# Optimization experiments

Hardware: AMD Instinct MI355X
Metric: run time of the kernel (lower is better)

## Reference

```python
import jax, jax.numpy as jnp
import numpy as np

N_ATOM = 10000
D = 256
N_EDGE = 160000
BN_EPS = 1e-6


def _bn_eval(x, g, b, m, v):
    # BatchNorm1d in eval mode
    return (x - m) * jax.lax.rsqrt(v + BN_EPS) * g + b


def setup_inputs() -> dict:
    key = jax.random.key(0)
    ks = jax.random.split(key, 12)
    def glorot(k, shape):
        fan_in = shape[-1]
        return jax.random.normal(k, shape, dtype=jnp.float32) / np.sqrt(fan_in)
    inp = {
        'atom': jax.random.normal(ks[0], (N_ATOM, D), dtype=jnp.float32),
        'bond_index': jax.random.randint(ks[1], (2, N_EDGE), 0, N_ATOM, dtype=jnp.int32),
        # align: Linear(2D -> 1) + BN(1)
        'W_align': glorot(ks[2], (1, 2 * D)),
        'b_align': jnp.zeros((1,), jnp.float32),
        'bn_a_g': jnp.ones((1,), jnp.float32),
        'bn_a_b': jnp.zeros((1,), jnp.float32),
        'bn_a_m': jnp.zeros((1,), jnp.float32),
        'bn_a_v': jnp.ones((1,), jnp.float32),
        # attend: Linear(D -> D) + BN(D)
        'W_att': glorot(ks[3], (D, D)),
        'b_att': jnp.zeros((D,), jnp.float32),
        'bn_t_g': jnp.ones((D,), jnp.float32),
        'bn_t_b': jnp.zeros((D,), jnp.float32),
        'bn_t_m': jnp.zeros((D,), jnp.float32),
        'bn_t_v': jnp.ones((D,), jnp.float32),
        # GRUCell(D, D): weights stacked [r; z; n] as in torch
        'W_ih': glorot(ks[4], (3 * D, D)),
        'W_hh': glorot(ks[5], (3 * D, D)),
        'b_ih': jnp.zeros((3 * D,), jnp.float32),
        'b_hh': jnp.zeros((3 * D,), jnp.float32),
    }
    return inp


def reference(atom, bond_index, W_align, b_align, bn_a_g, bn_a_b, bn_a_m, bn_a_v,
              W_att, b_att, bn_t_g, bn_t_b, bn_t_m, bn_t_v,
              W_ih, W_hh, b_ih, b_hh):
    num_atom = atom.shape[0]
    src = bond_index[0]
    dst = bond_index[1]

    # gather + concat: [E, 2D]
    feat_align = jnp.concatenate([atom[src], atom[dst]], axis=-1)
    # align score: Linear(2D->1) + BN + leaky_relu -> [E, 1]
    s = feat_align @ W_align.T + b_align
    s = _bn_eval(s, bn_a_g, bn_a_b, bn_a_m, bn_a_v)
    s = jax.nn.leaky_relu(s, negative_slope=0.01)

    # segment softmax over edges grouped by src atom
    seg_max = jax.ops.segment_max(s, src, num_segments=num_atom)  # [N, 1]
    e = jnp.exp(s - seg_max[src])
    denom = jax.ops.segment_sum(e, src, num_segments=num_atom)    # [N, 1]
    attn = e / (denom[src] + 1e-8)                                # [E, 1]

    # attend: Linear(D->D) + BN on gathered dst features
    h = atom[dst] @ W_att.T + b_att
    h = _bn_eval(h, bn_t_g, bn_t_b, bn_t_m, bn_t_v)

    # weighted scatter-add aggregation -> [N, D], then ELU
    context = jax.ops.segment_sum(attn * h, src, num_segments=num_atom)
    context = jax.nn.elu(context)

    # GRUCell: input=context, hidden=atom
    gi = context @ W_ih.T + b_ih   # [N, 3D]
    gh = atom @ W_hh.T + b_hh      # [N, 3D]
    i_r, i_z, i_n = jnp.split(gi, 3, axis=-1)
    h_r, h_z, h_n = jnp.split(gh, 3, axis=-1)
    r = jax.nn.sigmoid(i_r + h_r)
    z = jax.nn.sigmoid(i_z + h_z)
    n = jnp.tanh(i_n + r * h_n)
    update = (1.0 - z) * n + z * atom
    return update
```

## Files before the change

### kernel.cpp

```cpp
#include <hip/hip_runtime.h>
#include <hip/hip_bf16.h>

#define D 256
#define CAP 64

typedef __attribute__((ext_vector_type(8))) short bf16x8;
typedef __attribute__((ext_vector_type(4))) short s16x4;
typedef __attribute__((ext_vector_type(4))) float f32x4;

#define MFMA __builtin_amdgcn_mfma_f32_16x16x32_bf16

__device__ __forceinline__ float s2f(short u) {
    union { unsigned int i; float f; } c;
    c.i = ((unsigned int)(unsigned short)u) << 16;
    return c.f;
}
__device__ __forceinline__ short f2s(float f) {
    union { float f; unsigned int u; } c; c.f = f;
    unsigned int u = c.u;
    u += 0x7fffu + ((u >> 16) & 1u);
    return (short)(u >> 16);
}

__global__ __launch_bounds__(256) void prep_kernel(
    const float* __restrict__ atom, short* __restrict__ atom_bf,
    const float* __restrict__ W_align, const float* __restrict__ b_align,
    const float* __restrict__ g, const float* __restrict__ bb,
    const float* __restrict__ mn, const float* __restrict__ vr,
    float* __restrict__ p0p, float* __restrict__ p1p,
    const float* __restrict__ Wa, short* __restrict__ Wa_bf,
    const float* __restrict__ Wi, short* __restrict__ Wi_bf,
    const float* __restrict__ Wh, short* __restrict__ Wh_bf,
    int* __restrict__ cnt,
    int N, int NROWB, int WCVTB)
{
    int b = blockIdx.x, tid = threadIdx.x;
    if (b < NROWB) {
        int wave = tid >> 6, lane = tid & 63;
        int row = b * 4 + wave;
        if (row >= N) return;
        float4 a = *(const float4*)(atom + (size_t)row * D + lane * 4);
        s16x4 o; o[0] = f2s(a.x); o[1] = f2s(a.y); o[2] = f2s(a.z); o[3] = f2s(a.w);
        ((s16x4*)(atom_bf + (size_t)row * D))[lane] = o;
        float4 w0 = *(const float4*)(W_align + lane * 4);
        float4 w1 = *(const float4*)(W_align + D + lane * 4);
        float d0 = a.x * w0.x + a.y * w0.y + a.z * w0.z + a.w * w0.w;
        float d1 = a.x * w1.x + a.y * w1.y + a.z * w1.z + a.w * w1.w;
        #pragma unroll
        for (int s = 32; s > 0; s >>= 1) {
            d0 += __shfl_xor(d0, s, 64);
            d1 += __shfl_xor(d1, s, 64);
        }
        if (lane == 0) {
            float A = rsqrtf(vr[0] + 1e-6f) * g[0];
            p0p[row] = A * (d0 + b_align[0]) + bb[0] - A * mn[0];
            p1p[row] = A * d1;
        }
        return;
    }
    b -= NROWB;
    if (b < WCVTB) {
        int nW4 = D * D / 4, nG4 = 3 * D * D / 4;
        int j = b * 256 + tid;
        const float* srcp; short* dstp;
        if (j < nW4) { srcp = Wa; dstp = Wa_bf; }
        else { j -= nW4;
            if (j < nG4) { srcp = Wi; dstp = Wi_bf; }
            else { j -= nG4;
                if (j < nG4) { srcp = Wh; dstp = Wh_bf; }
                else return;
            }
        }
        float4 v = ((const float4*)srcp)[j];
        s16x4 o; o[0] = f2s(v.x); o[1] = f2s(v.y); o[2] = f2s(v.z); o[3] = f2s(v.w);
        ((s16x4*)dstp)[j] = o;
        return;
    }
    b -= WCVTB;
    int i = b * 256 + tid;
    if (i < N) cnt[i] = 0;
}

__global__ __launch_bounds__(256) void fill_hA_kernel(
    const int* __restrict__ src, const int* __restrict__ dst,
    int* __restrict__ cnt, int* __restrict__ dlist, int E, int EB,
    const short* __restrict__ atom_bf, const short* __restrict__ W_bf,
    const float* __restrict__ bias,
    const float* __restrict__ g, const float* __restrict__ bb,
    const float* __restrict__ mn, const float* __restrict__ vr,
    short* __restrict__ hA, int N, int NB)
{
    int tid = threadIdx.x;
    if ((int)blockIdx.x < EB) {
        int e = blockIdx.x * 256 + tid;
        if (e < E) {
            int s = src[e];
            int p = atomicAdd(&cnt[s], 1);
            if (p < CAP) dlist[(s << 6) + p] = dst[e];
        }
        return;
    }
    __shared__ short Bs[2048 * 8];
    int bi = blockIdx.x - EB;
    int xcd = bi & 7, rest = bi >> 3;
    int cb = rest & 3, gh = rest >> 2;
    int gg = gh * 8 + xcd;
    if (gg >= NB) return;
    int c0 = cb * 64;
    for (int c = tid; c < 2048; c += 256) {
        int l15c = c & 15, quadc = (c >> 4) & 3, t2 = c >> 6;
        int kkc = t2 & 7, jc = t2 >> 3;
        bf16x8 v = *(const bf16x8*)(W_bf + (size_t)(c0 + jc * 16 + l15c) * D + quadc * 8 + kkc * 32);
        *(bf16x8*)(&Bs[c * 8]) = v;
    }
    __syncthreads();

    int wave = tid >> 6, lane = tid & 63;
    int quad = lane >> 4, l15 = lane & 15;
    int m0 = gg * 128 + wave * 16;
    int ar0 = m0 + l15;       if (ar0 > N - 1) ar0 = N - 1;
    int ar1 = m0 + 64 + l15;  if (ar1 > N - 1) ar1 = N - 1;
    const short* ap0 = atom_bf + (size_t)ar0 * D + quad * 8;
    const short* ap1 = atom_bf + (size_t)ar1 * D + quad * 8;
    const short* lb = &Bs[lane * 8];
    f32x4 acc[2][4];
    #pragma unroll
    for (int t = 0; t < 2; t++)
        #pragma unroll
        for (int j = 0; j < 4; j++) acc[t][j] = (f32x4){0,0,0,0};
    #pragma unroll
    for (int kk = 0; kk < 8; kk++) {
        int k = kk * 32;
        bf16x8 a0 = *(const bf16x8*)(ap0 + k);
        bf16x8 a1 = *(const bf16x8*)(ap1 + k);
        bf16x8 b0 = *(const bf16x8*)(lb + (0 * 8 + kk) * 512);
        bf16x8 b1 = *(const bf16x8*)(lb + (1 * 8 + kk) * 512);
        bf16x8 b2 = *(const bf16x8*)(lb + (2 * 8 + kk) * 512);
        bf16x8 b3 = *(const bf16x8*)(lb + (3 * 8 + kk) * 512);
        acc[0][0] = MFMA(a0, b0, acc[0][0], 0, 0, 0);
        acc[0][1] = MFMA(a0, b1, acc[0][1], 0, 0, 0);
        acc[0][2] = MFMA(a0, b2, acc[0][2], 0, 0, 0);
        acc[0][3] = MFMA(a0, b3, acc[0][3], 0, 0, 0);
        acc[1][0] = MFMA(a1, b0, acc[1][0], 0, 0, 0);
        acc[1][1] = MFMA(a1, b1, acc[1][1], 0, 0, 0);
        acc[1][2] = MFMA(a1, b2, acc[1][2], 0, 0, 0);
        acc[1][3] = MFMA(a1, b3, acc[1][3], 0, 0, 0);
    }
    #pragma unroll
    for (int j = 0; j < 4; j++) {
        int col = c0 + j * 16 + l15;
        float sc = rsqrtf(vr[col] + 1e-6f) * g[col];
        float sh = bb[col] - mn[col] * sc;
        float bi_ = bias[col];
        #pragma unroll
        for (int t = 0; t < 2; t++) {
            #pragma unroll
            for (int r = 0; r < 4; r++) {
                int row = m0 + t * 64 + quad * 4 + r;
                if (row < N) hA[(size_t)row * D + col] = f2s((acc[t][j][r] + bi_) * sc + sh);
            }
        }
    }
}

__global__ __launch_bounds__(256) void agg_kernel(
    const int* __restrict__ cnt, const int* __restrict__ dlist,
    const float* __restrict__ p0p, const float* __restrict__ p1p,
    const short* __restrict__ hA, short* __restrict__ ctx, int N)
{
    int w = (blockIdx.x * blockDim.x + threadIdx.x) >> 6;
    int lane = threadIdx.x & 63;
    if (w >= N) return;
    int deg = cnt[w]; if (deg > CAP) deg = CAP;
    int base = w << 6;
    float u = p0p[w];
    int grp = lane >> 4, l16 = lane & 15;
    float acc[16];
    #pragma unroll
    for (int i = 0; i < 16; i++) acc[i] = 0.f;
    float se = 0.f;
    for (int j = grp; j < deg; j += 4) {
        int d = dlist[base + j];
        float x = u + p1p[d];
        x = x > 0.f ? x : 0.01f * x;
        float e = __expf(x);
        se += e;
        const short* hp = hA + (size_t)d * D + l16 * 16;
        bf16x8 h0 = *(const bf16x8*)(hp);
        bf16x8 h1 = *(const bf16x8*)(hp + 8);
        #pragma unroll
        for (int i = 0; i < 8; i++) acc[i]     += e * s2f(h0[i]);
        #pragma unroll
        for (int i = 0; i < 8; i++) acc[8 + i] += e * s2f(h1[i]);
    }
    se += __shfl_xor(se, 16, 64);
    se += __shfl_xor(se, 32, 64);
    #pragma unroll
    for (int i = 0; i < 16; i++) {
        acc[i] += __shfl_xor(acc[i], 16, 64);
        acc[i] += __shfl_xor(acc[i], 32, 64);
    }
    if (grp == 0) {
        float inv = 1.f / (se + 1e-8f);
        bf16x8 o0, o1;
        #pragma unroll
        for (int i = 0; i < 8; i++) {
            float v0 = acc[i] * inv;
            v0 = v0 > 0.f ? v0 : __expf(v0) - 1.f;
            o0[i] = f2s(v0);
            float v1 = acc[8 + i] * inv;
            v1 = v1 > 0.f ? v1 : __expf(v1) - 1.f;
            o1[i] = f2s(v1);
        }
        short* cp = ctx + (size_t)w * D + l16 * 16;
        *(bf16x8*)cp = o0;
        *(bf16x8*)(cp + 8) = o1;
    }
}

__global__ __launch_bounds__(256) void gru_kernel(
    const short* __restrict__ ctx, const short* __restrict__ atom_bf,
    const short* __restrict__ W_ih, const short* __restrict__ W_hh,
    const float* __restrict__ b_ih, const float* __restrict__ b_hh,
    float* __restrict__ out, int N, int NB)
{
    __shared__ short Bs[3072 * 8];
    int bi = blockIdx.x;
    int xcd = bi & 7, rest = bi >> 3;
    int cb = rest & 15, gh = rest >> 4;
    int gg = gh * 8 + xcd;
    if (gg >= NB) return;
    int c0 = cb * 16;
    int tid = threadIdx.x;
    for (int c = tid; c < 3072; c += 256) {
        int l15c = c & 15, quadc = (c >> 4) & 3, t2 = c >> 6;
        int kkc = t2 & 7, gate = t2 >> 3;
        const short* srcp = (gate < 3)
            ? W_ih + (size_t)(gate * 256 + c0 + l15c) * D + quadc * 8 + kkc * 32
            : W_hh + (size_t)((gate - 3) * 256 + c0 + l15c) * D + quadc * 8 + kkc * 32;
        *(bf16x8*)(&Bs[c * 8]) = *(const bf16x8*)srcp;
    }
    __syncthreads();

    int wave = tid >> 6, lane = tid & 63;
    int quad = lane >> 4, l15 = lane & 15;
    int m0 = gg * 128 + wave * 16;
    int ar0 = m0 + l15;       if (ar0 > N - 1) ar0 = N - 1;
    int ar1 = m0 + 64 + l15;  if (ar1 > N - 1) ar1 = N - 1;
    const short* cp0 = ctx + (size_t)ar0 * D + quad * 8;
    const short* ap0 = atom_bf + (size_t)ar0 * D + quad * 8;
    const short* cp1 = ctx + (size_t)ar1 * D + quad * 8;
    const short* ap1 = atom_bf + (size_t)ar1 * D + quad * 8;
    const short* lb = &Bs[lane * 8];
    f32x4 gi[2][3], gh_[2][3];
    #pragma unroll
    for (int t = 0; t < 2; t++)
        #pragma unroll
        for (int j = 0; j < 3; j++) { gi[t][j] = (f32x4){0,0,0,0}; gh_[t][j] = (f32x4){0,0,0,0}; }
    #pragma unroll
    for (int kk = 0; kk < 8; kk++) {
        int k = kk * 32;
        bf16x8 c0v = *(const bf16x8*)(cp0 + k);
        bf16x8 a0v = *(const bf16x8*)(ap0 + k);
        bf16x8 c1v = *(const bf16x8*)(cp1 + k);
        bf16x8 a1v = *(const bf16x8*)(ap1 + k);
        bf16x8 bir = *(const bf16x8*)(lb + (0 * 8 + kk) * 512);
        bf16x8 biz = *(const bf16x8*)(lb + (1 * 8 + kk) * 512);
        bf16x8 bin = *(const bf16x8*)(lb + (2 * 8 + kk) * 512);
        bf16x8 bhr = *(const bf16x8*)(lb + (3 * 8 + kk) * 512);
        bf16x8 bhz = *(const bf16x8*)(lb + (4 * 8 + kk) * 512);
        bf16x8 bhn = *(const bf16x8*)(lb + (5 * 8 + kk) * 512);
        gi[0][0] = MFMA(c0v, bir, gi[0][0], 0, 0, 0);
        gi[0][1] = MFMA(c0v, biz, gi[0][1], 0, 0, 0);
        gi[0][2] = MFMA(c0v, bin, gi[0][2], 0, 0, 0);
        gh_[0][0] = MFMA(a0v, bhr, gh_[0][0], 0, 0, 0);
        gh_[0][1] = MFMA(a0v, bhz, gh_[0][1], 0, 0, 0);
        gh_[0][2] = MFMA(a0v, bhn, gh_[0][2], 0, 0, 0);
        gi[1][0] = MFMA(c1v, bir, gi[1][0], 0, 0, 0);
        gi[1][1] = MFMA(c1v, biz, gi[1][1], 0, 0, 0);
        gi[1][2] = MFMA(c1v, bin, gi[1][2], 0, 0, 0);
        gh_[1][0] = MFMA(a1v, bhr, gh_[1][0], 0, 0, 0);
        gh_[1][1] = MFMA(a1v, bhz, gh_[1][1], 0, 0, 0);
        gh_[1][2] = MFMA(a1v, bhn, gh_[1][2], 0, 0, 0);
    }
    int col = c0 + l15;
    float bir_s = b_ih[col], biz_s = b_ih[col + 256], bin_s = b_ih[col + 512];
    float bhr_s = b_hh[col], bhz_s = b_hh[col + 256], bhn_s = b_hh[col + 512];
    #pragma unroll
    for (int t = 0; t < 2; t++) {
        #pragma unroll
        for (int r = 0; r < 4; r++) {
            int row = m0 + t * 64 + quad * 4 + r;
            if (row < N) {
                float rr = 1.f / (1.f + __expf(-(gi[t][0][r] + bir_s + gh_[t][0][r] + bhr_s)));
                float zz = 1.f / (1.f + __expf(-(gi[t][1][r] + biz_s + gh_[t][1][r] + bhz_s)));
                float nn = tanhf(gi[t][2][r] + bin_s + rr * (gh_[t][2][r] + bhn_s));
                float at = s2f(atom_bf[(size_t)row * D + col]);
                out[(size_t)row * D + col] = (1.f - zz) * nn + zz * at;
            }
        }
    }
}

extern "C" void kernel_launch(void* const* d_in, const int* in_sizes, int n_in,
                              void* d_out, int out_size, void* d_ws, size_t ws_size,
                              hipStream_t stream) {
    const float* atom    = (const float*)d_in[0];
    const int*   bond    = (const int*)d_in[1];
    const float* W_align = (const float*)d_in[2];
    const float* b_align = (const float*)d_in[3];
    const float* bn_a_g  = (const float*)d_in[4];
    const float* bn_a_b  = (const float*)d_in[5];
    const float* bn_a_m  = (const float*)d_in[6];
    const float* bn_a_v  = (const float*)d_in[7];
    const float* W_att   = (const float*)d_in[8];
    const float* b_att   = (const float*)d_in[9];
    const float* bn_t_g  = (const float*)d_in[10];
    const float* bn_t_b  = (const float*)d_in[11];
    const float* bn_t_m  = (const float*)d_in[12];
    const float* bn_t_v  = (const float*)d_in[13];
    const float* W_ih    = (const float*)d_in[14];
    const float* W_hh    = (const float*)d_in[15];
    const float* b_ih    = (const float*)d_in[16];
    const float* b_hh    = (const float*)d_in[17];

    int N = in_sizes[0] / D;
    int E = in_sizes[1] / 2;
    const int* src = bond;
    const int* dst = bond + E;

    char* w = (char*)d_ws;
    size_t o = 0;
    auto alloc = [&](size_t bytes) {
        void* p = w + o;
        o = (o + bytes + 255) & ~(size_t)255;
        return p;
    };
    int*   cnt     = (int*)alloc((size_t)N * 4);
    int*   dlist   = (int*)alloc((size_t)N * CAP * 4);
    float* p0p     = (float*)alloc((size_t)N * 4);
    float* p1p     = (float*)alloc((size_t)N * 4);
    short* hA      = (short*)alloc((size_t)N * D * 2);
    short* ctx     = (short*)alloc((size_t)N * D * 2);
    short* atom_bf = (short*)alloc((size_t)N * D * 2);
    short* Watt_bf = (short*)alloc((size_t)D * D * 2);
    short* Wih_bf  = (short*)alloc((size_t)3 * D * D * 2);
    short* Whh_bf  = (short*)alloc((size_t)3 * D * D * 2);

    int NROWB = (N + 3) / 4;
    int nWtot4 = (D * D + 2 * 3 * D * D) / 4;
    int WCVTB = (nWtot4 + 255) / 256;
    int ZB = (N + 255) / 256;
    int EB = (E + 255) / 256;
    int NB = (N + 127) / 128;
    int GH = (NB + 7) / 8;

    prep_kernel<<<NROWB + WCVTB + ZB, 256, 0, stream>>>(
        atom, atom_bf, W_align, b_align, bn_a_g, bn_a_b, bn_a_m, bn_a_v, p0p, p1p,
        W_att, Watt_bf, W_ih, Wih_bf, W_hh, Whh_bf, cnt, N, NROWB, WCVTB);
    fill_hA_kernel<<<EB + 8 * 4 * GH, 256, 0, stream>>>(
        src, dst, cnt, dlist, E, EB,
        atom_bf, Watt_bf, b_att, bn_t_g, bn_t_b, bn_t_m, bn_t_v, hA, N, NB);
    agg_kernel<<<((size_t)N * 64 + 255) / 256, 256, 0, stream>>>(
        cnt, dlist, p0p, p1p, hA, ctx, N);
    gru_kernel<<<8 * 16 * GH, 256, 0, stream>>>(
        ctx, atom_bf, Wih_bf, Whh_bf, b_ih, b_hh, (float*)d_out, N, NB);
}
```

Before: 163.7 us.

## Drop separate bf16 prep pass; convert fp32 on the fly inside GEMM kernels

Removes the prep kernel that wrote bf16 copies of atom and the weight matrices. The hA GEMM, edge-list fill and align projection now run as three block ranges of one kernel, and the GEMMs read fp32 atom and weights and convert them to bf16 as they load. The count array is zeroed with hipMemsetAsync instead of prep blocks. This saves a launch and a full write-and-read pass over the bf16 atom buffer, but the GEMM kernels load twice the bytes per operand and every block repeats the weight conversion.

```diff
diff --git a/kernel.cpp b/kernel.cpp
--- a/kernel.cpp
+++ b/kernel.cpp
@@ -21,78 +21,96 @@
     u += 0x7fffu + ((u >> 16) & 1u);
     return (short)(u >> 16);
 }
-
-__global__ __launch_bounds__(256) void prep_kernel(
-    const float* __restrict__ atom, short* __restrict__ atom_bf,
+__device__ __forceinline__ bf16x8 cvt8(const float* p) {
+    float4 f0 = *(const float4*)p;
+    float4 f1 = *(const float4*)(p + 4);
+    bf16x8 r;
+    r[0] = f2s(f0.x); r[1] = f2s(f0.y); r[2] = f2s(f0.z); r[3] = f2s(f0.w);
+    r[4] = f2s(f1.x); r[5] = f2s(f1.y); r[6] = f2s(f1.z); r[7] = f2s(f1.w);
+    return r;
+}
+
+__global__ __launch_bounds__(256) void k1_kernel(
+    const float* __restrict__ atom,
+    const float* __restrict__ W_att, const float* __restrict__ bias,
+    const float* __restrict__ g_t, const float* __restrict__ bb_t,
+    const float* __restrict__ mn_t, const float* __restrict__ vr_t,
+    short* __restrict__ hA,
+    const int* __restrict__ src, const int* __restrict__ dst,
+    int* __restrict__ cnt, int* __restrict__ dlist,
     const float* __restrict__ W_align, const float* __restrict__ b_align,
-    const float* __restrict__ g, const float* __restrict__ bb,
-    const float* __restrict__ mn, const float* __restrict__ vr,
+    const float* __restrict__ g_a, const float* __restrict__ bb_a,
+    const float* __restrict__ mn_a, const float* __restrict__ vr_a,
     float* __restrict__ p0p, float* __restrict__ p1p,
-    const float* __restrict__ Wa, short* __restrict__ Wa_bf,
-    const float* __restrict__ Wi, short* __restrict__ Wi_bf,
-    const float* __restrict__ Wh, short* __restrict__ Wh_bf,
-    int* __restrict__ cnt,
-    int N, int NROWB, int WCVTB)
-{
-    int b = blockIdx.x, tid = threadIdx.x;
-    if (b < NROWB) {
-        int wave = tid >> 6, lane = tid & 63;
-        int row = b * 4 + wave;
-        if (row >= N) return;
-        float4 a = *(const float4*)(atom + (size_t)row * D + lane * 4);
-        s16x4 o; o[0] = f2s(a.x); o[1] = f2s(a.y); o[2] = f2s(a.z); o[3] = f2s(a.w);
-        ((s16x4*)(atom_bf + (size_t)row * D))[lane] = o;
-        float4 w0 = *(const float4*)(W_align + lane * 4);
-        float4 w1 = *(const float4*)(W_align + D + lane * 4);
-        float d0 = a.x * w0.x + a.y * w0.y + a.z * w0.z + a.w * w0.w;
-        float d1 = a.x * w1.x + a.y * w1.y + a.z * w1.z + a.w * w1.w;
-        #pragma unroll
-        for (int s = 32; s > 0; s >>= 1) {
-            d0 += __shfl_xor(d0, s, 64);
-            d1 += __shfl_xor(d1, s, 64);
-        }
-        if (lane == 0) {
-            float A = rsqrtf(vr[0] + 1e-6f) * g[0];
-            p0p[row] = A * (d0 + b_align[0]) + bb[0] - A * mn[0];
-            p1p[row] = A * d1;
-        }
-        return;
-    }
-    b -= NROWB;
-    if (b < WCVTB) {
-        int nW4 = D * D / 4, nG4 = 3 * D * D / 4;
-        int j = b * 256 + tid;
-        const float* srcp; short* dstp;
-        if (j < nW4) { srcp = Wa; dstp = Wa_bf; }
-        else { j -= nW4;
-            if (j < nG4) { srcp = Wi; dstp = Wi_bf; }
-            else { j -= nG4;
-                if (j < nG4) { srcp = Wh; dstp = Wh_bf; }
-                else return;
-            }
-        }
-        float4 v = ((const float4*)srcp)[j];
-        s16x4 o; o[0] = f2s(v.x); o[1] = f2s(v.y); o[2] = f2s(v.z); o[3] = f2s(v.w);
-        ((s16x4*)dstp)[j] = o;
-        return;
-    }
-    b -= WCVTB;
-    int i = b * 256 + tid;
-    if (i < N) cnt[i] = 0;
-}
-
-__global__ __launch_bounds__(256) void fill_hA_kernel(
-    const int* __restrict__ src, const int* __restrict__ dst,
-    int* __restrict__ cnt, int* __restrict__ dlist, int E, int EB,
-    const short* __restrict__ atom_bf, const short* __restrict__ W_bf,
-    const float* __restrict__ bias,
-    const float* __restrict__ g, const float* __restrict__ bb,
-    const float* __restrict__ mn, const float* __restrict__ vr,
-    short* __restrict__ hA, int N, int NB)
+    int N, int E, int NB, int HB, int FB)
 {
     int tid = threadIdx.x;
-    if ((int)blockIdx.x < EB) {
-        int e = blockIdx.x * 256 + tid;
+    int b = blockIdx.x;
+    if (b < HB) {
+        __shared__ short Bs[2048 * 8];
+        int xcd = b & 7, rest = b >> 3;
+        int cb = rest & 3, gh = rest >> 2;
+        int gg = gh * 8 + xcd;
+        if (gg >= NB) return;
+        int c0 = cb * 64;
+        for (int c = tid; c < 2048; c += 256) {
+            int l15c = c & 15, quadc = (c >> 4) & 3, t2 = c >> 6;
+            int kkc = t2 & 7, jc = t2 >> 3;
+            *(bf16x8*)(&Bs[c * 8]) =
+                cvt8(W_att + (size_t)(c0 + jc * 16 + l15c) * D + quadc * 8 + kkc * 32);
+        }
+        __syncthreads();
+
+        int wave = tid >> 6, lane = tid & 63;
+        int quad = lane >> 4, l15 = lane & 15;
+        int m0 = gg * 128 + wave * 16;
+        int ar0 = m0 + l15;       if (ar0 > N - 1) ar0 = N - 1;
+        int ar1 = m0 + 64 + l15;  if (ar1 > N - 1) ar1 = N - 1;
+        const float* ap0 = atom + (size_t)ar0 * D + quad * 8;
+        const float* ap1 = atom + (size_t)ar1 * D + quad * 8;
+        const short* lb = &Bs[lane * 8];
+        f32x4 acc[2][4];
+        #pragma unroll
+        for (int t = 0; t < 2; t++)
+            #pragma unroll
+            for (int j = 0; j < 4; j++) acc[t][j] = (f32x4){0,0,0,0};
+        #pragma unroll
+        for (int kk = 0; kk < 8; kk++) {
+            bf16x8 a0 = cvt8(ap0 + kk * 32);
+            bf16x8 a1 = cvt8(ap1 + kk * 32);
+            bf16x8 b0 = *(const bf16x8*)(lb + (0 * 8 + kk) * 512);
+            bf16x8 b1 = *(const bf16x8*)(lb + (1 * 8 + kk) * 512);
+            bf16x8 b2 = *(const bf16x8*)(lb + (2 * 8 + kk) * 512);
+            bf16x8 b3 = *(const bf16x8*)(lb + (3 * 8 + kk) * 512);
+            acc[0][0] = MFMA(a0, b0, acc[0][0], 0, 0, 0);
+            acc[0][1] = MFMA(a0, b1, acc[0][1], 0, 0, 0);
+            acc[0][2] = MFMA(a0, b2, acc[0][2], 0, 0, 0);
+            acc[0][3] = MFMA(a0, b3, acc[0][3], 0, 0, 0);
+            acc[1][0] = MFMA(a1, b0, acc[1][0], 0, 0, 0);
+            acc[1][1] = MFMA(a1, b1, acc[1][1], 0, 0, 0);
+            acc[1][2] = MFMA(a1, b2, acc[1][2], 0, 0, 0);
+            acc[1][3] = MFMA(a1, b3, acc[1][3], 0, 0, 0);
+        }
+        #pragma unroll
+        for (int j = 0; j < 4; j++) {
+            int col = c0 + j * 16 + l15;
+            float sc = rsqrtf(vr_t[col] + 1e-6f) * g_t[col];
+            float sh = bb_t[col] - mn_t[col] * sc;
+            float bi_ = bias[col];
+            #pragma unroll
+            for (int t = 0; t < 2; t++) {
+                #pragma unroll
+                for (int r = 0; r < 4; r++) {
+                    int row = m0 + t * 64 + quad * 4 + r;
+                    if (row < N) hA[(size_t)row * D + col] = f2s((acc[t][j][r] + bi_) * sc + sh);
+                }
+            }
+        }
+        return;
+    }
+    b -= HB;
+    if (b < FB) {
+        int e = b * 256 + tid;
         if (e < E) {
             int s = src[e];
             int p = atomicAdd(&cnt[s], 1);
@@ -100,66 +118,24 @@
         }
         return;
     }
-    __shared__ short Bs[2048 * 8];
-    int bi = blockIdx.x - EB;
-    int xcd = bi & 7, rest = bi >> 3;
-    int cb = rest & 3, gh = rest >> 2;
-    int gg = gh * 8 + xcd;
-    if (gg >= NB) return;
-    int c0 = cb * 64;
-    for (int c = tid; c < 2048; c += 256) {
-        int l15c = c & 15, quadc = (c >> 4) & 3, t2 = c >> 6;
-        int kkc = t2 & 7, jc = t2 >> 3;
-        bf16x8 v = *(const bf16x8*)(W_bf + (size_t)(c0 + jc * 16 + l15c) * D + quadc * 8 + kkc * 32);
-        *(bf16x8*)(&Bs[c * 8]) = v;
-    }
-    __syncthreads();
-
+    b -= FB;
     int wave = tid >> 6, lane = tid & 63;
-    int quad = lane >> 4, l15 = lane & 15;
-    int m0 = gg * 128 + wave * 16;
-    int ar0 = m0 + l15;       if (ar0 > N - 1) ar0 = N - 1;
-    int ar1 = m0 + 64 + l15;  if (ar1 > N - 1) ar1 = N - 1;
-    const short* ap0 = atom_bf + (size_t)ar0 * D + quad * 8;
-    const short* ap1 = atom_bf + (size_t)ar1 * D + quad * 8;
-    const short* lb = &Bs[lane * 8];
-    f32x4 acc[2][4];
-    #pragma unroll
-    for (int t = 0; t < 2; t++)
-        #pragma unroll
-        for (int j = 0; j < 4; j++) acc[t][j] = (f32x4){0,0,0,0};
-    #pragma unroll
-    for (int kk = 0; kk < 8; kk++) {
-        int k = kk * 32;
-        bf16x8 a0 = *(const bf16x8*)(ap0 + k);
-        bf16x8 a1 = *(const bf16x8*)(ap1 + k);
-        bf16x8 b0 = *(const bf16x8*)(lb + (0 * 8 + kk) * 512);
-        bf16x8 b1 = *(const bf16x8*)(lb + (1 * 8 + kk) * 512);
-        bf16x8 b2 = *(const bf16x8*)(lb + (2 * 8 + kk) * 512);
-        bf16x8 b3 = *(const bf16x8*)(lb + (3 * 8 + kk) * 512);
-        acc[0][0] = MFMA(a0, b0, acc[0][0], 0, 0, 0);
-        acc[0][1] = MFMA(a0, b1, acc[0][1], 0, 0, 0);
-        acc[0][2] = MFMA(a0, b2, acc[0][2], 0, 0, 0);
-        acc[0][3] = MFMA(a0, b3, acc[0][3], 0, 0, 0);
-        acc[1][0] = MFMA(a1, b0, acc[1][0], 0, 0, 0);
-        acc[1][1] = MFMA(a1, b1, acc[1][1], 0, 0, 0);
-        acc[1][2] = MFMA(a1, b2, acc[1][2], 0, 0, 0);
-        acc[1][3] = MFMA(a1, b3, acc[1][3], 0, 0, 0);
-    }
-    #pragma unroll
-    for (int j = 0; j < 4; j++) {
-        int col = c0 + j * 16 + l15;
-        float sc = rsqrtf(vr[col] + 1e-6f) * g[col];
-        float sh = bb[col] - mn[col] * sc;
-        float bi_ = bias[col];
-        #pragma unroll
-        for (int t = 0; t < 2; t++) {
-            #pragma unroll
-            for (int r = 0; r < 4; r++) {
-                int row = m0 + t * 64 + quad * 4 + r;
-                if (row < N) hA[(size_t)row * D + col] = f2s((acc[t][j][r] + bi_) * sc + sh);
-            }
-        }
+    int row = b * 4 + wave;
+    if (row >= N) return;
+    float4 a = *(const float4*)(atom + (size_t)row * D + lane * 4);
+    float4 w0 = *(const float4*)(W_align + lane * 4);
+    float4 w1 = *(const float4*)(W_align + D + lane * 4);
+    float d0 = a.x * w0.x + a.y * w0.y + a.z * w0.z + a.w * w0.w;
+    float d1 = a.x * w1.x + a.y * w1.y + a.z * w1.z + a.w * w1.w;
+    #pragma unroll
+    for (int s = 32; s > 0; s >>= 1) {
+        d0 += __shfl_xor(d0, s, 64);
+        d1 += __shfl_xor(d1, s, 64);
+    }
+    if (lane == 0) {
+        float A = rsqrtf(vr_a[0] + 1e-6f) * g_a[0];
+        p0p[row] = A * (d0 + b_align[0]) + bb_a[0] - A * mn_a[0];
+        p1p[row] = A * d1;
     }
 }
 
@@ -219,8 +195,8 @@
 }
 
 __global__ __launch_bounds__(256) void gru_kernel(
-    const short* __restrict__ ctx, const short* __restrict__ atom_bf,
-    const short* __restrict__ W_ih, const short* __restrict__ W_hh,
+    const short* __restrict__ ctx, const float* __restrict__ atom,
+    const float* __restrict__ W_ih, const float* __restrict__ W_hh,
     const float* __restrict__ b_ih, const float* __restrict__ b_hh,
     float* __restrict__ out, int N, int NB)
 {
@@ -235,10 +211,10 @@
     for (int c = tid; c < 3072; c += 256) {
         int l15c = c & 15, quadc = (c >> 4) & 3, t2 = c >> 6;
         int kkc = t2 & 7, gate = t2 >> 3;
-        const short* srcp = (gate < 3)
+        const float* srcp = (gate < 3)
             ? W_ih + (size_t)(gate * 256 + c0 + l15c) * D + quadc * 8 + kkc * 32
             : W_hh + (size_t)((gate - 3) * 256 + c0 + l15c) * D + quadc * 8 + kkc * 32;
-        *(bf16x8*)(&Bs[c * 8]) = *(const bf16x8*)srcp;
+        *(bf16x8*)(&Bs[c * 8]) = cvt8(srcp);
     }
     __syncthreads();
 
@@ -248,9 +224,9 @@
     int ar0 = m0 + l15;       if (ar0 > N - 1) ar0 = N - 1;
     int ar1 = m0 + 64 + l15;  if (ar1 > N - 1) ar1 = N - 1;
     const short* cp0 = ctx + (size_t)ar0 * D + quad * 8;
-    const short* ap0 = atom_bf + (size_t)ar0 * D + quad * 8;
+    const float* ap0 = atom + (size_t)ar0 * D + quad * 8;
     const short* cp1 = ctx + (size_t)ar1 * D + quad * 8;
-    const short* ap1 = atom_bf + (size_t)ar1 * D + quad * 8;
+    const float* ap1 = atom + (size_t)ar1 * D + quad * 8;
     const short* lb = &Bs[lane * 8];
     f32x4 gi[2][3], gh_[2][3];
     #pragma unroll
@@ -261,9 +237,9 @@
     for (int kk = 0; kk < 8; kk++) {
         int k = kk * 32;
         bf16x8 c0v = *(const bf16x8*)(cp0 + k);
-        bf16x8 a0v = *(const bf16x8*)(ap0 + k);
+        bf16x8 a0v = cvt8(ap0 + k);
         bf16x8 c1v = *(const bf16x8*)(cp1 + k);
-        bf16x8 a1v = *(const bf16x8*)(ap1 + k);
+        bf16x8 a1v = cvt8(ap1 + k);
         bf16x8 bir = *(const bf16x8*)(lb + (0 * 8 + kk) * 512);
         bf16x8 biz = *(const bf16x8*)(lb + (1 * 8 + kk) * 512);
         bf16x8 bin = *(const bf16x8*)(lb + (2 * 8 + kk) * 512);
@@ -295,7 +271,7 @@
                 float rr = 1.f / (1.f + __expf(-(gi[t][0][r] + bir_s + gh_[t][0][r] + bhr_s)));
                 float zz = 1.f / (1.f + __expf(-(gi[t][1][r] + biz_s + gh_[t][1][r] + bhz_s)));
                 float nn = tanhf(gi[t][2][r] + bin_s + rr * (gh_[t][2][r] + bhn_s));
-                float at = s2f(atom_bf[(size_t)row * D + col]);
+                float at = atom[(size_t)row * D + col];
                 out[(size_t)row * D + col] = (1.f - zz) * nn + zz * at;
             }
         }
@@ -336,33 +312,27 @@
         o = (o + bytes + 255) & ~(size_t)255;
         return p;
     };
-    int*   cnt     = (int*)alloc((size_t)N * 4);
-    int*   dlist   = (int*)alloc((size_t)N * CAP * 4);
-    float* p0p     = (float*)alloc((size_t)N * 4);
-    float* p1p     = (float*)alloc((size_t)N * 4);
-    short* hA      = (short*)alloc((size_t)N * D * 2);
-    short* ctx     = (short*)alloc((size_t)N * D * 2);
-    short* atom_bf = (short*)alloc((size_t)N * D * 2);
-    short* Watt_bf = (short*)alloc((size_t)D * D * 2);
-    short* Wih_bf  = (short*)alloc((size_t)3 * D * D * 2);
-    short* Whh_bf  = (short*)alloc((size_t)3 * D * D * 2);
-
-    int NROWB = (N + 3) / 4;
-    int nWtot4 = (D * D + 2 * 3 * D * D) / 4;
-    int WCVTB = (nWtot4 + 255) / 256;
-    int ZB = (N + 255) / 256;
-    int EB = (E + 255) / 256;
+    int*   cnt   = (int*)alloc((size_t)N * 4);
+    int*   dlist = (int*)alloc((size_t)N * CAP * 4);
+    float* p0p   = (float*)alloc((size_t)N * 4);
+    float* p1p   = (float*)alloc((size_t)N * 4);
+    short* hA    = (short*)alloc((size_t)N * D * 2);
+    short* ctx   = (short*)alloc((size_t)N * D * 2);
+
     int NB = (N + 127) / 128;
     int GH = (NB + 7) / 8;
-
-    prep_kernel<<<NROWB + WCVTB + ZB, 256, 0, stream>>>(
-        atom, atom_bf, W_align, b_align, bn_a_g, bn_a_b, bn_a_m, bn_a_v, p0p, p1p,
-        W_att, Watt_bf, W_ih, Wih_bf, W_hh, Whh_bf, cnt, N, NROWB, WCVTB);
-    fill_hA_kernel<<<EB + 8 * 4 * GH, 256, 0, stream>>>(
-        src, dst, cnt, dlist, E, EB,
-        atom_bf, Watt_bf, b_att, bn_t_g, bn_t_b, bn_t_m, bn_t_v, hA, N, NB);
+    int HB = 8 * 4 * GH;
+    int FB = (E + 255) / 256;
+    int PB = (N + 3) / 4;
+
+    hipMemsetAsync(cnt, 0, (size_t)N * 4, stream);
+    k1_kernel<<<HB + FB + PB, 256, 0, stream>>>(
+        atom, W_att, b_att, bn_t_g, bn_t_b, bn_t_m, bn_t_v, hA,
+        src, dst, cnt, dlist,
+        W_align, b_align, bn_a_g, bn_a_b, bn_a_m, bn_a_v, p0p, p1p,
+        N, E, NB, HB, FB);
     agg_kernel<<<((size_t)N * 64 + 255) / 256, 256, 0, stream>>>(
         cnt, dlist, p0p, p1p, hA, ctx, N);
     gru_kernel<<<8 * 16 * GH, 256, 0, stream>>>(
-        ctx, atom_bf, Wih_bf, Whh_bf, b_ih, b_hh, (float*)d_out, N, NB);
-}
+        ctx, atom, W_ih, W_hh, b_ih, b_hh, (float*)d_out, N, NB);
+}
```

Result: slower. 179.4 us (+9.6%).

## Pre-swizzle bf16 weights into MFMA fragment layout and read B operands directly from global

Applied to the files above, without the earlier changes.

The prep kernel now writes the attend and GRU weights in bf16 already arranged in the per-lane MFMA B-fragment order. The GEMM kernels drop their shared-memory staging and barrier and load B fragments straight from global memory, relying on L2/L1 caching. The XCD-aware block remapping is removed and the GEMM blocks are placed ahead of the edge-scatter blocks in the fused launch. This trades LDS staging cost for repeated global/cache reads of the weights per block.

```diff
diff --git a/kernel.cpp b/kernel.cpp
--- a/kernel.cpp
+++ b/kernel.cpp
@@ -21,6 +21,15 @@
     u += 0x7fffu + ((u >> 16) & 1u);
     return (short)(u >> 16);
 }
+__device__ __forceinline__ bf16x8 cvt8(const float* p) {
+    float4 f0 = *(const float4*)p;
+    float4 f1 = *(const float4*)(p + 4);
+    bf16x8 r;
+    r[0] = f2s(f0.x); r[1] = f2s(f0.y); r[2] = f2s(f0.z); r[3] = f2s(f0.w);
+    r[4] = f2s(f1.x); r[5] = f2s(f1.y); r[6] = f2s(f1.z); r[7] = f2s(f1.w);
+    return r;
+}
+
 
 __global__ __launch_bounds__(256) void prep_kernel(
     const float* __restrict__ atom, short* __restrict__ atom_bf,
@@ -28,9 +37,9 @@
     const float* __restrict__ g, const float* __restrict__ bb,
     const float* __restrict__ mn, const float* __restrict__ vr,
     float* __restrict__ p0p, float* __restrict__ p1p,
-    const float* __restrict__ Wa, short* __restrict__ Wa_bf,
-    const float* __restrict__ Wi, short* __restrict__ Wi_bf,
-    const float* __restrict__ Wh, short* __restrict__ Wh_bf,
+    const float* __restrict__ Wa, short* __restrict__ WaR,
+    const float* __restrict__ Wi, const float* __restrict__ Wh,
+    short* __restrict__ WgR,
     int* __restrict__ cnt,
     int N, int NROWB, int WCVTB)
 {
@@ -60,20 +69,27 @@
     }
     b -= NROWB;
     if (b < WCVTB) {
-        int nW4 = D * D / 4, nG4 = 3 * D * D / 4;
         int j = b * 256 + tid;
-        const float* srcp; short* dstp;
-        if (j < nW4) { srcp = Wa; dstp = Wa_bf; }
-        else { j -= nW4;
-            if (j < nG4) { srcp = Wi; dstp = Wi_bf; }
-            else { j -= nG4;
-                if (j < nG4) { srcp = Wh; dstp = Wh_bf; }
-                else return;
+        if (j < 8192) {
+            int cb = j >> 11, r = j & 2047;
+            int jj = r >> 9, r2 = r & 511;
+            int kk = r2 >> 6, lane = r2 & 63;
+            int q = lane >> 4, l15 = lane & 15;
+            const float* src = Wa + (size_t)(cb * 64 + jj * 16 + l15) * D + q * 8 + kk * 32;
+            *(bf16x8*)(WaR + (size_t)j * 8) = cvt8(src);
+        } else {
+            int j2 = j - 8192;
+            if (j2 < 49152) {
+                int cb = j2 / 3072, r = j2 - cb * 3072;
+                int gate = r >> 9, r2 = r & 511;
+                int kk = r2 >> 6, lane = r2 & 63;
+                int q = lane >> 4, l15 = lane & 15;
+                const float* srcp = (gate < 3)
+                    ? Wi + (size_t)(gate * 256 + cb * 16 + l15) * D + q * 8 + kk * 32
+                    : Wh + (size_t)((gate - 3) * 256 + cb * 16 + l15) * D + q * 8 + kk * 32;
+                *(bf16x8*)(WgR + (size_t)j2 * 8) = cvt8(srcp);
             }
         }
-        float4 v = ((const float4*)srcp)[j];
-        s16x4 o; o[0] = f2s(v.x); o[1] = f2s(v.y); o[2] = f2s(v.z); o[3] = f2s(v.w);
-        ((s16x4*)dstp)[j] = o;
         return;
     }
     b -= WCVTB;
@@ -83,16 +99,16 @@
 
 __global__ __launch_bounds__(256) void fill_hA_kernel(
     const int* __restrict__ src, const int* __restrict__ dst,
-    int* __restrict__ cnt, int* __restrict__ dlist, int E, int EB,
-    const short* __restrict__ atom_bf, const short* __restrict__ W_bf,
+    int* __restrict__ cnt, int* __restrict__ dlist, int E, int HB,
+    const short* __restrict__ atom_bf, const short* __restrict__ WaR,
     const float* __restrict__ bias,
     const float* __restrict__ g, const float* __restrict__ bb,
     const float* __restrict__ mn, const float* __restrict__ vr,
-    short* __restrict__ hA, int N, int NB)
+    short* __restrict__ hA, int N)
 {
     int tid = threadIdx.x;
-    if ((int)blockIdx.x < EB) {
-        int e = blockIdx.x * 256 + tid;
+    if ((int)blockIdx.x >= HB) {
+        int e = (blockIdx.x - HB) * 256 + tid;
         if (e < E) {
             int s = src[e];
             int p = atomicAdd(&cnt[s], 1);
@@ -100,21 +116,9 @@
         }
         return;
     }
-    __shared__ short Bs[2048 * 8];
-    int bi = blockIdx.x - EB;
-    int xcd = bi & 7, rest = bi >> 3;
-    int cb = rest & 3, gh = rest >> 2;
-    int gg = gh * 8 + xcd;
-    if (gg >= NB) return;
+    int bi = blockIdx.x;
+    int cb = bi & 3, gg = bi >> 2;
     int c0 = cb * 64;
-    for (int c = tid; c < 2048; c += 256) {
-        int l15c = c & 15, quadc = (c >> 4) & 3, t2 = c >> 6;
-        int kkc = t2 & 7, jc = t2 >> 3;
-        bf16x8 v = *(const bf16x8*)(W_bf + (size_t)(c0 + jc * 16 + l15c) * D + quadc * 8 + kkc * 32);
-        *(bf16x8*)(&Bs[c * 8]) = v;
-    }
-    __syncthreads();
-
     int wave = tid >> 6, lane = tid & 63;
     int quad = lane >> 4, l15 = lane & 15;
     int m0 = gg * 128 + wave * 16;
@@ -122,7 +126,7 @@
     int ar1 = m0 + 64 + l15;  if (ar1 > N - 1) ar1 = N - 1;
     const short* ap0 = atom_bf + (size_t)ar0 * D + quad * 8;
     const short* ap1 = atom_bf + (size_t)ar1 * D + quad * 8;
-    const short* lb = &Bs[lane * 8];
+    const short* lb = WaR + (size_t)cb * 16384 + lane * 8;
     f32x4 acc[2][4];
     #pragma unroll
     for (int t = 0; t < 2; t++)
@@ -220,30 +224,17 @@
 
 __global__ __launch_bounds__(256) void gru_kernel(
     const short* __restrict__ ctx, const short* __restrict__ atom_bf,
-    const short* __restrict__ W_ih, const short* __restrict__ W_hh,
+    const short* __restrict__ WgR,
     const float* __restrict__ b_ih, const float* __restrict__ b_hh,
-    float* __restrict__ out, int N, int NB)
+    float* __restrict__ out, int N)
 {
-    __shared__ short Bs[3072 * 8];
     int bi = blockIdx.x;
-    int xcd = bi & 7, rest = bi >> 3;
-    int cb = rest & 15, gh = rest >> 4;
-    int gg = gh * 8 + xcd;
-    if (gg >= NB) return;
+    int cb = bi & 15, gg = bi >> 4;
     int c0 = cb * 16;
     int tid = threadIdx.x;
-    for (int c = tid; c < 3072; c += 256) {
-        int l15c = c & 15, quadc = (c >> 4) & 3, t2 = c >> 6;
-        int kkc = t2 & 7, gate = t2 >> 3;
-        const short* srcp = (gate < 3)
-            ? W_ih + (size_t)(gate * 256 + c0 + l15c) * D + quadc * 8 + kkc * 32
-            : W_hh + (size_t)((gate - 3) * 256 + c0 + l15c) * D + quadc * 8 + kkc * 32;
-        *(bf16x8*)(&Bs[c * 8]) = *(const bf16x8*)srcp;
-    }
-    __syncthreads();
-
     int wave = tid >> 6, lane = tid & 63;
     int quad = lane >> 4, l15 = lane & 15;
+    const short* lb = WgR + (size_t)cb * 24576 + lane * 8;
     int m0 = gg * 128 + wave * 16;
     int ar0 = m0 + l15;       if (ar0 > N - 1) ar0 = N - 1;
     int ar1 = m0 + 64 + l15;  if (ar1 > N - 1) ar1 = N - 1;
@@ -251,7 +242,6 @@
     const short* ap0 = atom_bf + (size_t)ar0 * D + quad * 8;
     const short* cp1 = ctx + (size_t)ar1 * D + quad * 8;
     const short* ap1 = atom_bf + (size_t)ar1 * D + quad * 8;
-    const short* lb = &Bs[lane * 8];
     f32x4 gi[2][3], gh_[2][3];
     #pragma unroll
     for (int t = 0; t < 2; t++)
@@ -343,26 +333,24 @@
     short* hA      = (short*)alloc((size_t)N * D * 2);
     short* ctx     = (short*)alloc((size_t)N * D * 2);
     short* atom_bf = (short*)alloc((size_t)N * D * 2);
-    short* Watt_bf = (short*)alloc((size_t)D * D * 2);
-    short* Wih_bf  = (short*)alloc((size_t)3 * D * D * 2);
-    short* Whh_bf  = (short*)alloc((size_t)3 * D * D * 2);
+    short* WaR     = (short*)alloc((size_t)8192 * 8 * 2);
+    short* WgR     = (short*)alloc((size_t)49152 * 8 * 2);
 
     int NROWB = (N + 3) / 4;
-    int nWtot4 = (D * D + 2 * 3 * D * D) / 4;
-    int WCVTB = (nWtot4 + 255) / 256;
+    int WCVTB = (8192 + 49152) / 256;
     int ZB = (N + 255) / 256;
     int EB = (E + 255) / 256;
     int NB = (N + 127) / 128;
-    int GH = (NB + 7) / 8;
+    int HB = 4 * NB;
 
     prep_kernel<<<NROWB + WCVTB + ZB, 256, 0, stream>>>(
         atom, atom_bf, W_align, b_align, bn_a_g, bn_a_b, bn_a_m, bn_a_v, p0p, p1p,
-        W_att, Watt_bf, W_ih, Wih_bf, W_hh, Whh_bf, cnt, N, NROWB, WCVTB);
-    fill_hA_kernel<<<EB + 8 * 4 * GH, 256, 0, stream>>>(
-        src, dst, cnt, dlist, E, EB,
-        atom_bf, Watt_bf, b_att, bn_t_g, bn_t_b, bn_t_m, bn_t_v, hA, N, NB);
+        W_att, WaR, W_ih, W_hh, WgR, cnt, N, NROWB, WCVTB);
+    fill_hA_kernel<<<HB + EB, 256, 0, stream>>>(
+        src, dst, cnt, dlist, E, HB,
+        atom_bf, WaR, b_att, bn_t_g, bn_t_b, bn_t_m, bn_t_v, hA, N);
     agg_kernel<<<((size_t)N * 64 + 255) / 256, 256, 0, stream>>>(
         cnt, dlist, p0p, p1p, hA, ctx, N);
-    gru_kernel<<<8 * 16 * GH, 256, 0, stream>>>(
-        ctx, atom_bf, Wih_bf, Whh_bf, b_ih, b_hh, (float*)d_out, N, NB);
-}
+    gru_kernel<<<16 * NB, 256, 0, stream>>>(
+        ctx, atom_bf, WgR, b_ih, b_hh, (float*)d_out, N);
+}
```

New measurement: 174.9 us. 1.07x slower.

## Stage weights via direct global-to-LDS loads and prefetch A operands in GRU

Applied to the files above, without the earlier changes.

Weight-tile staging in the attend and GRU kernels now uses global_load_lds to write straight into shared memory without a register round trip. The GRU kernel issues its first A-operand loads before the weight staging and prefetches the next k-slice inside the MFMA loop. The aggregation kernel computes each edge's exp score once per lane and broadcasts index and weight with shuffles, so per-edge dlist and p1p loads are no longer repeated inside the gather loop. These changes add register pressure and rely on the global_load_lds builtin's layout semantics.

```diff
diff --git a/kernel.cpp b/kernel.cpp
--- a/kernel.cpp
+++ b/kernel.cpp
@@ -20,6 +20,12 @@
     unsigned int u = c.u;
     u += 0x7fffu + ((u >> 16) & 1u);
     return (short)(u >> 16);
+}
+__device__ __forceinline__ void ld16_lds(void* lds, const void* gsrc) {
+    __builtin_amdgcn_global_load_lds(
+        (const __attribute__((address_space(1))) unsigned int*)gsrc,
+        (__attribute__((address_space(3))) unsigned int*)lds,
+        16, 0, 0);
 }
 
 __global__ __launch_bounds__(256) void prep_kernel(
@@ -107,11 +113,13 @@
     int gg = gh * 8 + xcd;
     if (gg >= NB) return;
     int c0 = cb * 64;
-    for (int c = tid; c < 2048; c += 256) {
+    #pragma unroll
+    for (int it = 0; it < 8; it++) {
+        int c = tid + it * 256;
         int l15c = c & 15, quadc = (c >> 4) & 3, t2 = c >> 6;
         int kkc = t2 & 7, jc = t2 >> 3;
-        bf16x8 v = *(const bf16x8*)(W_bf + (size_t)(c0 + jc * 16 + l15c) * D + quadc * 8 + kkc * 32);
-        *(bf16x8*)(&Bs[c * 8]) = v;
+        ld16_lds(&Bs[c * 8],
+                 W_bf + (size_t)(c0 + jc * 16 + l15c) * D + quadc * 8 + kkc * 32);
     }
     __syncthreads();
 
@@ -173,28 +181,36 @@
     if (w >= N) return;
     int deg = cnt[w]; if (deg > CAP) deg = CAP;
     int base = w << 6;
-    float u = p0p[w];
+    int d = 0; float e = 0.f;
+    if (lane < deg) {
+        d = dlist[base + lane];
+        float x = p0p[w] + p1p[d];
+        x = x > 0.f ? x : 0.01f * x;
+        e = __expf(x);
+    }
+    float se = e;
+    #pragma unroll
+    for (int s = 32; s > 0; s >>= 1) se += __shfl_xor(se, s, 64);
+
     int grp = lane >> 4, l16 = lane & 15;
     float acc[16];
     #pragma unroll
     for (int i = 0; i < 16; i++) acc[i] = 0.f;
-    float se = 0.f;
-    for (int j = grp; j < deg; j += 4) {
-        int d = dlist[base + j];
-        float x = u + p1p[d];
-        x = x > 0.f ? x : 0.01f * x;
-        float e = __expf(x);
-        se += e;
-        const short* hp = hA + (size_t)d * D + l16 * 16;
+    int nit = (deg + 3) >> 2;
+    for (int it = 0; it < nit; ++it) {
+        int j = it * 4 + grp;
+        int jc = j < deg ? j : 0;
+        int dj = __shfl(d, jc, 64);
+        float ej = __shfl(e, jc, 64);
+        if (j >= deg) ej = 0.f;
+        const short* hp = hA + (size_t)dj * D + l16 * 16;
         bf16x8 h0 = *(const bf16x8*)(hp);
         bf16x8 h1 = *(const bf16x8*)(hp + 8);
         #pragma unroll
-        for (int i = 0; i < 8; i++) acc[i]     += e * s2f(h0[i]);
-        #pragma unroll
-        for (int i = 0; i < 8; i++) acc[8 + i] += e * s2f(h1[i]);
-    }
-    se += __shfl_xor(se, 16, 64);
-    se += __shfl_xor(se, 32, 64);
+        for (int i = 0; i < 8; i++) acc[i]     += ej * s2f(h0[i]);
+        #pragma unroll
+        for (int i = 0; i < 8; i++) acc[8 + i] += ej * s2f(h1[i]);
+    }
     #pragma unroll
     for (int i = 0; i < 16; i++) {
         acc[i] += __shfl_xor(acc[i], 16, 64);
@@ -232,15 +248,6 @@
     if (gg >= NB) return;
     int c0 = cb * 16;
     int tid = threadIdx.x;
-    for (int c = tid; c < 3072; c += 256) {
-        int l15c = c & 15, quadc = (c >> 4) & 3, t2 = c >> 6;
-        int kkc = t2 & 7, gate = t2 >> 3;
-        const short* srcp = (gate < 3)
-            ? W_ih + (size_t)(gate * 256 + c0 + l15c) * D + quadc * 8 + kkc * 32
-            : W_hh + (size_t)((gate - 3) * 256 + c0 + l15c) * D + quadc * 8 + kkc * 32;
-        *(bf16x8*)(&Bs[c * 8]) = *(const bf16x8*)srcp;
-    }
-    __syncthreads();
 
     int wave = tid >> 6, lane = tid & 63;
     int quad = lane >> 4, l15 = lane & 15;
@@ -251,6 +258,24 @@
     const short* ap0 = atom_bf + (size_t)ar0 * D + quad * 8;
     const short* cp1 = ctx + (size_t)ar1 * D + quad * 8;
     const short* ap1 = atom_bf + (size_t)ar1 * D + quad * 8;
+
+    bf16x8 c0v = *(const bf16x8*)(cp0);
+    bf16x8 a0v = *(const bf16x8*)(ap0);
+    bf16x8 c1v = *(const bf16x8*)(cp1);
+    bf16x8 a1v = *(const bf16x8*)(ap1);
+
+    #pragma unroll
+    for (int it = 0; it < 12; it++) {
+        int c = tid + it * 256;
+        int l15c = c & 15, quadc = (c >> 4) & 3, t2 = c >> 6;
+        int kkc = t2 & 7, gate = t2 >> 3;
+        const short* srcp = (gate < 3)
+            ? W_ih + (size_t)(gate * 256 + c0 + l15c) * D + quadc * 8 + kkc * 32
+            : W_hh + (size_t)((gate - 3) * 256 + c0 + l15c) * D + quadc * 8 + kkc * 32;
+        ld16_lds(&Bs[c * 8], srcp);
+    }
+    __syncthreads();
+
     const short* lb = &Bs[lane * 8];
     f32x4 gi[2][3], gh_[2][3];
     #pragma unroll
@@ -259,11 +284,14 @@
         for (int j = 0; j < 3; j++) { gi[t][j] = (f32x4){0,0,0,0}; gh_[t][j] = (f32x4){0,0,0,0}; }
     #pragma unroll
     for (int kk = 0; kk < 8; kk++) {
-        int k = kk * 32;
-        bf16x8 c0v = *(const bf16x8*)(cp0 + k);
-        bf16x8 a0v = *(const bf16x8*)(ap0 + k);
-        bf16x8 c1v = *(const bf16x8*)(cp1 + k);
-        bf16x8 a1v = *(const bf16x8*)(ap1 + k);
+        bf16x8 nc0, na0, nc1, na1;
+        if (kk < 7) {
+            int k = (kk + 1) * 32;
+            nc0 = *(const bf16x8*)(cp0 + k);
+            na0 = *(const bf16x8*)(ap0 + k);
+            nc1 = *(const bf16x8*)(cp1 + k);
+            na1 = *(const bf16x8*)(ap1 + k);
+        }
         bf16x8 bir = *(const bf16x8*)(lb + (0 * 8 + kk) * 512);
         bf16x8 biz = *(const bf16x8*)(lb + (1 * 8 + kk) * 512);
         bf16x8 bin = *(const bf16x8*)(lb + (2 * 8 + kk) * 512);
@@ -282,6 +310,7 @@
         gh_[1][0] = MFMA(a1v, bhr, gh_[1][0], 0, 0, 0);
         gh_[1][1] = MFMA(a1v, bhz, gh_[1][1], 0, 0, 0);
         gh_[1][2] = MFMA(a1v, bhn, gh_[1][2], 0, 0, 0);
+        if (kk < 7) { c0v = nc0; a0v = na0; c1v = nc1; a1v = na1; }
     }
     int col = c0 + l15;
     float bir_s = b_ih[col], biz_s = b_ih[col + 256], bin_s = b_ih[col + 512];
```

Measured after the change: 164.9 us. No clear change (+0.7%).
